# Kernel tuning notes

Measured on AMD Instinct MI355X. Metric: run time of the kernel, lower is better.

The kernel has to match this reference:

```python
import jax, jax.numpy as jnp
import numpy as np

B, S, D, H = 8, 1024, 1024, 16
HD = D // H  # 64


def setup_inputs() -> dict:
    key = jax.random.key(0)
    ks = jax.random.split(key, 10)
    s = 1.0 / np.sqrt(HD)
    x = jax.random.normal(ks[0], (B, S, D), dtype=jnp.float32)
    mask = jax.random.randint(ks[1], (B, S), 0, 2).astype(bool)  # True = padded
    # per-head q/k/v projections of SimpleAttention, stacked over heads
    Wq = jax.random.normal(ks[2], (H, HD, HD), dtype=jnp.float32) * s
    bq = jnp.zeros((H, HD), dtype=jnp.float32)
    Wk = jax.random.normal(ks[3], (H, HD, HD), dtype=jnp.float32) * s
    bk = jnp.zeros((H, HD), dtype=jnp.float32)
    Wv = jax.random.normal(ks[4], (H, HD, HD), dtype=jnp.float32) * s
    bv = jnp.zeros((H, HD), dtype=jnp.float32)
    # out_proj: Linear(dim, dim)
    Wo = jax.random.normal(ks[5], (D, D), dtype=jnp.float32) * (1.0 / np.sqrt(D))
    bo = jnp.zeros((D,), dtype=jnp.float32)
    return {"x": x, "mask": mask, "Wq": Wq, "bq": bq, "Wk": Wk, "bk": bk,
            "Wv": Wv, "bv": bv, "Wo": Wo, "bo": bo}


def reference(x, mask, Wq, bq, Wk, bk, Wv, bv, Wo, bo):
    b, s, d = x.shape
    xh = x.reshape(b, s, H, HD).transpose(0, 2, 1, 3)  # (b, h, s, hd)
    # per-head linear projections (batched over heads via einsum)
    q = jnp.einsum('bhsd,hde->bhse', xh, Wq) + bq[None, :, None, :]
    k = jnp.einsum('bhsd,hde->bhse', xh, Wk) + bk[None, :, None, :]
    v = jnp.einsum('bhsd,hde->bhse', xh, Wv) + bv[None, :, None, :]
    scale = 1.0 / jnp.sqrt(jnp.asarray(HD, dtype=x.dtype))
    scores = jnp.einsum('bhqd,bhkd->bhqk', q, k) * scale  # (b, h, s, s)
    # key-padding mask: True = padded -> -inf on key axis
    neg = jnp.asarray(jnp.finfo(x.dtype).min, dtype=x.dtype)
    scores = jnp.where(mask[:, None, None, :], neg, scores)
    attn = jax.nn.softmax(scores, axis=-1)
    out = jnp.einsum('bhqk,bhkd->bhqd', attn, v)  # (b, h, s, hd)
    concat = out.transpose(0, 2, 1, 3).reshape(b, s, d)
    # out_proj (dropout is identity in eval)
    return concat @ Wo.T + bo
```

## Files before the change

kernel.cpp:

```cpp
#include <hip/hip_runtime.h>
#include <float.h>

#define B_ 8
#define S_ 1024
#define D_ 1024
#define H_ 16
#define HD_ 64

typedef __attribute__((ext_vector_type(8))) _Float16 half8;
typedef __attribute__((ext_vector_type(4))) _Float16 half4;
typedef __attribute__((ext_vector_type(4))) float f32x4;

__device__ __forceinline__ void gld16(const void* g, void* l) {
  __builtin_amdgcn_global_load_lds(
      (const __attribute__((address_space(1))) void*)g,
      (__attribute__((address_space(3))) void*)l, 16, 0, 0);
}

__global__ void detect_mask_kernel(const unsigned int* __restrict__ m, int* __restrict__ flag) {
  __shared__ int bad;
  if (threadIdx.x == 0) bad = 0;
  __syncthreads();
  int my = 0;
  for (int i = threadIdx.x; i < 2048; i += 256) {
    if (m[i] & ~1u) my = 1;
  }
  if (my) atomicOr(&bad, 1);
  __syncthreads();
  if (threadIdx.x == 0) *flag = bad;
}

__global__ void expand_mask_kernel(const unsigned char* __restrict__ mb,
                                   const int* __restrict__ mi,
                                   const int* __restrict__ flag,
                                   float* __restrict__ maskadd) {
  int i = blockIdx.x * 256 + threadIdx.x;
  if (i < B_ * S_) {
    int f = *flag;
    int v = f ? (int)mb[i] : mi[i];
    maskadd[i] = (v != 0) ? -FLT_MAX : 0.0f;
  }
}

__global__ void cast_wo_kernel(const float* __restrict__ Wo, _Float16* __restrict__ Wo16) {
  int i = blockIdx.x * 256 + threadIdx.x;
  if (i < D_ * D_) Wo16[i] = (_Float16)Wo[i];
}

__global__ void cast_wqkv_kernel(const float* __restrict__ Wq, const float* __restrict__ bq,
                                 const float* __restrict__ Wk, const float* __restrict__ bk,
                                 const float* __restrict__ Wv, const float* __restrict__ bv,
                                 _Float16* __restrict__ Wc, float* __restrict__ bs) {
  int idx = blockIdx.x * 256 + threadIdx.x;
  if (idx < 16 * 3 * 64 * 64) {
    int d = idx & 63;
    int e = (idx >> 6) & 63;
    int t2 = idx >> 12;
    int m = t2 % 3, h = t2 / 3;
    int src = h * 4096 + d * 64 + e;
    float v = (m == 0) ? Wq[src] * 0.18033688f : (m == 1) ? Wk[src] : Wv[src];
    Wc[idx] = (_Float16)v;
  }
  if (idx < 3072) {
    int m = idx >> 10, he = idx & 1023;
    float v = (m == 0) ? bq[he] * 0.18033688f : (m == 1) ? bk[he] : bv[he];
    bs[idx] = v;
  }
}

__global__ __launch_bounds__(256) void qkv_kernel(
    const float* __restrict__ x, const _Float16* __restrict__ Wc,
    const float* __restrict__ bs,
    _Float16* __restrict__ q16, _Float16* __restrict__ k16, _Float16* __restrict__ vT16) {
  const int tile = blockIdx.x & 15;
  const int bh = blockIdx.x >> 4;
  const int b = bh >> 4, h = bh & 15;
  const int s0 = tile * 64;
  const int w = threadIdx.x >> 6, lane = threadIdx.x & 63;
  const int col = lane & 15, quad = lane >> 4;
  const int srow = s0 + w * 16 + col;

  const float* xr = x + ((size_t)(b * S_) + srow) * D_ + h * HD_;
  f32x4 x0a = *(const f32x4*)(xr + quad * 8);
  f32x4 x0b = *(const f32x4*)(xr + quad * 8 + 4);
  f32x4 x1a = *(const f32x4*)(xr + 32 + quad * 8);
  f32x4 x1b = *(const f32x4*)(xr + 32 + quad * 8 + 4);
  half8 Xf0, Xf1;
#pragma unroll
  for (int j = 0; j < 4; ++j) {
    Xf0[j] = (_Float16)x0a[j];
    Xf0[4 + j] = (_Float16)x0b[j];
    Xf1[j] = (_Float16)x1a[j];
    Xf1[4 + j] = (_Float16)x1b[j];
  }

  const _Float16* wbase = Wc + (size_t)h * 3 * 4096;
  const f32x4 z4 = {0.f, 0.f, 0.f, 0.f};
#pragma unroll
  for (int mm = 0; mm < 2; ++mm) {
    _Float16* outp = mm ? k16 : q16;
    const _Float16* wm = wbase + mm * 4096;
#pragma unroll
    for (int et = 0; et < 4; ++et) {
      const _Float16* wr = wm + (et * 16 + col) * 64;
      half8 W0 = *(const half8*)(wr + quad * 8);
      half8 W1 = *(const half8*)(wr + 32 + quad * 8);
      f32x4 c = __builtin_amdgcn_mfma_f32_16x16x32_f16(W0, Xf0, z4, 0, 0, 0);
      c = __builtin_amdgcn_mfma_f32_16x16x32_f16(W1, Xf1, c, 0, 0, 0);
      f32x4 bb = *(const f32x4*)(bs + mm * 1024 + h * 64 + et * 16 + quad * 4);
      half4 o;
#pragma unroll
      for (int r = 0; r < 4; ++r) o[r] = (_Float16)(c[r] + bb[r]);
      *(half4*)(outp + ((size_t)bh * S_ + srow) * HD_ + et * 16 + quad * 4) = o;
    }
  }
  {
    const _Float16* wm = wbase + 2 * 4096;
#pragma unroll
    for (int et = 0; et < 4; ++et) {
      const _Float16* wr = wm + (et * 16 + col) * 64;
      half8 W0 = *(const half8*)(wr + quad * 8);
      half8 W1 = *(const half8*)(wr + 32 + quad * 8);
      f32x4 c = __builtin_amdgcn_mfma_f32_16x16x32_f16(Xf0, W0, z4, 0, 0, 0);
      c = __builtin_amdgcn_mfma_f32_16x16x32_f16(Xf1, W1, c, 0, 0, 0);
      float bb = bs[2048 + h * 64 + et * 16 + col];
      half4 o;
#pragma unroll
      for (int r = 0; r < 4; ++r) o[r] = (_Float16)(c[r] + bb);
      *(half4*)(vT16 + ((size_t)bh * HD_ + et * 16 + col) * S_ + s0 + w * 16 + quad * 4) = o;
    }
  }
}

__global__ __launch_bounds__(256, 4) void attn_kernel(
    const _Float16* __restrict__ q, const _Float16* __restrict__ k,
    const _Float16* __restrict__ vT, const float* __restrict__ maskadd,
    _Float16* __restrict__ att) {
  __shared__ alignas(16) _Float16 Ks[2][64 * 64];
  __shared__ alignas(16) _Float16 Vs[2][64 * 64];
  const int bh = blockIdx.x & 127;
  const int qblk = blockIdx.x >> 7;
  const int b = bh >> 4, h = bh & 15;
  const int wv = threadIdx.x >> 6;
  const int lane = threadIdx.x & 63;
  const int quad = lane >> 4, col = lane & 15;
  const int c7 = col & 7;
  const int q0 = qblk * 128 + wv * 32;

  const _Float16* __restrict__ kb = k + (size_t)bh * S_ * HD_;
  const _Float16* __restrict__ vb = vT + (size_t)bh * HD_ * S_;
  const float* __restrict__ mrow = maskadd + b * S_;

  const int jj0 = wv * 128 + lane, jj1 = jj0 + 64;
  const int r0s = jj0 >> 3, r1s = jj1 >> 3;
  const int sg0 = (jj0 & 7) ^ (r0s & 7), sg1 = (jj1 & 7) ^ (r1s & 7);
  const int offK0 = r0s * 128 + sg0 * 16, offK1 = r1s * 128 + sg1 * 16;
  const int offV0 = r0s * 2048 + sg0 * 16, offV1 = r1s * 2048 + sg1 * 16;
  const int ldsb0 = wv * 1024, ldsb1 = wv * 1024 + 512;

  half8 Qf[2][2];
#pragma unroll
  for (int qt = 0; qt < 2; ++qt) {
    const _Float16* qrow = q + ((size_t)bh * S_ + q0 + qt * 16 + col) * HD_;
    Qf[qt][0] = *(const half8*)(qrow + quad * 8);
    Qf[qt][1] = *(const half8*)(qrow + 32 + quad * 8);
  }

  const f32x4 z4 = {0.f, 0.f, 0.f, 0.f};
  f32x4 O[2][4];
#pragma unroll
  for (int qt = 0; qt < 2; ++qt)
#pragma unroll
    for (int et = 0; et < 4; ++et) O[qt][et] = z4;
  float l[2] = {0.f, 0.f};

  {
    const char* kg = (const char*)kb;
    const char* vg = (const char*)vb;
    gld16(kg + offK0, &Ks[0][ldsb0]);
    gld16(kg + offK1, &Ks[0][ldsb1]);
    gld16(vg + offV0, &Vs[0][ldsb0]);
    gld16(vg + offV1, &Vs[0][ldsb1]);
  }
  int cur = 0;
  for (int c = 0; c < 16; ++c) {
    __syncthreads();
    if (c < 15) {
      const char* kg = (const char*)kb + (size_t)(c + 1) * 8192;
      const char* vg = (const char*)vb + (size_t)(c + 1) * 128;
      gld16(kg + offK0, &Ks[cur ^ 1][ldsb0]);
      gld16(kg + offK1, &Ks[cur ^ 1][ldsb1]);
      gld16(vg + offV0, &Vs[cur ^ 1][ldsb0]);
      gld16(vg + offV1, &Vs[cur ^ 1][ldsb1]);
    }
    const int kk0 = c * 64;
    const _Float16* Kb_ = &Ks[cur][0];
    const _Float16* Vb_ = &Vs[cur][0];
    f32x4 mkv[4];
#pragma unroll
    for (int kt = 0; kt < 4; ++kt) mkv[kt] = *(const f32x4*)(mrow + kk0 + kt * 16 + quad * 4);
    half8 Kf[4][2];
#pragma unroll
    for (int kt = 0; kt < 4; ++kt) {
      const int rb = (kt * 16 + col) * 64;
      Kf[kt][0] = *(const half8*)&Kb_[rb + ((quad) ^ c7) * 8];
      Kf[kt][1] = *(const half8*)&Kb_[rb + ((4 + quad) ^ c7) * 8];
    }
    f32x4 st[2][4];
#pragma unroll
    for (int qt = 0; qt < 2; ++qt)
#pragma unroll
      for (int kt = 0; kt < 4; ++kt) {
        f32x4 s = __builtin_amdgcn_mfma_f32_16x16x32_f16(Kf[kt][0], Qf[qt][0], mkv[kt], 0, 0, 0);
        st[qt][kt] = __builtin_amdgcn_mfma_f32_16x16x32_f16(Kf[kt][1], Qf[qt][1], s, 0, 0, 0);
      }
    half4 Vf[4][4];
#pragma unroll
    for (int kt = 0; kt < 4; ++kt) {
      const int sb = ((kt * 2 + (quad >> 1)) ^ c7) * 8 + (quad & 1) * 4;
#pragma unroll
      for (int et = 0; et < 4; ++et) Vf[kt][et] = *(const half4*)&Vb_[(et * 16 + col) * 64 + sb];
    }
#pragma unroll
    for (int qt = 0; qt < 2; ++qt) {
      float p[16];
#pragma unroll
      for (int kt = 0; kt < 4; ++kt)
#pragma unroll
        for (int r = 0; r < 4; ++r) p[kt * 4 + r] = __builtin_amdgcn_exp2f(st[qt][kt][r]);
      float s01 = (p[0] + p[1]) + (p[2] + p[3]);
      float s23 = (p[4] + p[5]) + (p[6] + p[7]);
      float s45 = (p[8] + p[9]) + (p[10] + p[11]);
      float s67 = (p[12] + p[13]) + (p[14] + p[15]);
      l[qt] += (s01 + s23) + (s45 + s67);
      half4 ph[4];
#pragma unroll
      for (int kt = 0; kt < 4; ++kt)
#pragma unroll
        for (int r = 0; r < 4; ++r) ph[kt][r] = (_Float16)p[kt * 4 + r];
#pragma unroll
      for (int et = 0; et < 4; ++et) {
        f32x4 o = O[qt][et];
#pragma unroll
        for (int kt = 0; kt < 4; ++kt)
          o = __builtin_amdgcn_mfma_f32_16x16x16f16(Vf[kt][et], ph[kt], o, 0, 0, 0);
        O[qt][et] = o;
      }
    }
    cur ^= 1;
  }
#pragma unroll
  for (int qt = 0; qt < 2; ++qt) {
    float lt = l[qt];
    lt += __shfl_xor(lt, 16);
    lt += __shfl_xor(lt, 32);
    const float inv = 1.0f / lt;
    _Float16* orow = att + ((size_t)(b * S_ + q0 + qt * 16 + col)) * D_ + h * HD_;
#pragma unroll
    for (int et = 0; et < 4; ++et) {
      half4 o;
#pragma unroll
      for (int r = 0; r < 4; ++r) o[r] = (_Float16)(O[qt][et][r] * inv);
      *(half4*)(orow + et * 16 + quad * 4) = o;
    }
  }
}

__global__ __launch_bounds__(256, 4) void outproj_kernel(
    const _Float16* __restrict__ A, const _Float16* __restrict__ Bw,
    const float* __restrict__ bo, float* __restrict__ C) {
  __shared__ alignas(16) _Float16 As[128 * 64];
  __shared__ alignas(16) _Float16 Bs[128 * 64];
  const int m0 = (int)(blockIdx.x >> 3) * 128;
  const int n0 = (int)(blockIdx.x & 7) * 128;
  const int t = threadIdx.x;
  const int lane = t & 63, wv = t >> 6;
  const int quad = lane >> 4, col = lane & 15;
  const int mw = (wv >> 1) * 64, nw = (wv & 1) * 64;

  int rowS[4], segS[4];
#pragma unroll
  for (int sweep = 0; sweep < 4; ++sweep) {
    const int s = sweep * 256 + wv * 64 + lane;
    rowS[sweep] = s >> 3;
    segS[sweep] = (s & 7) ^ (rowS[sweep] & 7);
  }

  f32x4 acc[16];
  const f32x4 z4 = {0.f, 0.f, 0.f, 0.f};
#pragma unroll
  for (int i = 0; i < 16; ++i) acc[i] = z4;

  for (int kt = 0; kt < 16; ++kt) {
#pragma unroll
    for (int sweep = 0; sweep < 4; ++sweep) {
      const int ldsbase = (sweep * 256 + wv * 64) * 8;
      gld16(A + (size_t)(m0 + rowS[sweep]) * D_ + kt * 64 + segS[sweep] * 8, &As[ldsbase]);
      gld16(Bw + (size_t)(n0 + rowS[sweep]) * D_ + kt * 64 + segS[sweep] * 8, &Bs[ldsbase]);
    }
    __syncthreads();
#pragma unroll
    for (int ks = 0; ks < 2; ++ks) {
      half8 aF[4], bF[4];
#pragma unroll
      for (int mt = 0; mt < 4; ++mt) {
        const int row = mw + mt * 16 + col;
        aF[mt] = *(const half8*)&As[row * 64 + (((ks * 4 + quad) ^ (row & 7)) * 8)];
      }
#pragma unroll
      for (int nt = 0; nt < 4; ++nt) {
        const int row = nw + nt * 16 + col;
        bF[nt] = *(const half8*)&Bs[row * 64 + (((ks * 4 + quad) ^ (row & 7)) * 8)];
      }
#pragma unroll
      for (int mt = 0; mt < 4; ++mt)
#pragma unroll
        for (int nt = 0; nt < 4; ++nt)
          acc[mt * 4 + nt] =
              __builtin_amdgcn_mfma_f32_16x16x32_f16(aF[mt], bF[nt], acc[mt * 4 + nt], 0, 0, 0);
    }
    __syncthreads();
  }
#pragma unroll
  for (int mt = 0; mt < 4; ++mt)
#pragma unroll
    for (int nt = 0; nt < 4; ++nt) {
      f32x4 a = acc[mt * 4 + nt];
      const int n = n0 + nw + nt * 16 + col;
      const float bb = bo[n];
#pragma unroll
      for (int r = 0; r < 4; ++r) {
        const int mrow = m0 + mw + mt * 16 + quad * 4 + r;
        C[(size_t)mrow * D_ + n] = a[r] + bb;
      }
    }
}

extern "C" void kernel_launch(void* const* d_in, const int* in_sizes, int n_in,
                              void* d_out, int out_size, void* d_ws, size_t ws_size,
                              hipStream_t stream) {
  const float* x  = (const float*)d_in[0];
  const float* Wq = (const float*)d_in[2];
  const float* bq = (const float*)d_in[3];
  const float* Wk = (const float*)d_in[4];
  const float* bk = (const float*)d_in[5];
  const float* Wv = (const float*)d_in[6];
  const float* bv = (const float*)d_in[7];
  const float* Wo = (const float*)d_in[8];
  const float* bo = (const float*)d_in[9];

  float* wsf     = (float*)d_ws;
  float* maskadd = wsf;
  int*   flag    = (int*)(wsf + 8192);
  const size_t NE = (size_t)B_ * H_ * S_ * HD_;
  _Float16* hws  = (_Float16*)(wsf + 16384);
  _Float16* q16  = hws;
  _Float16* k16  = q16 + NE;
  _Float16* vT16 = k16 + NE;
  _Float16* att16 = vT16 + NE;
  _Float16* Wo16 = att16 + NE;
  _Float16* Wc   = Wo16 + 1048576;
  float*    bs   = (float*)(Wc + 196608);

  detect_mask_kernel<<<1, 256, 0, stream>>>((const unsigned int*)d_in[1], flag);
  expand_mask_kernel<<<(B_ * S_ + 255) / 256, 256, 0, stream>>>(
      (const unsigned char*)d_in[1], (const int*)d_in[1], flag, maskadd);
  cast_wo_kernel<<<(D_ * D_ + 255) / 256, 256, 0, stream>>>(Wo, Wo16);
  cast_wqkv_kernel<<<(16 * 3 * 64 * 64 + 255) / 256, 256, 0, stream>>>(
      Wq, bq, Wk, bk, Wv, bv, Wc, bs);
  qkv_kernel<<<B_ * H_ * (S_ / 64), 256, 0, stream>>>(x, Wc, bs, q16, k16, vT16);
  attn_kernel<<<B_ * H_ * (S_ / 128), 256, 0, stream>>>(q16, k16, vT16, maskadd, att16);
  outproj_kernel<<<(B_ * S_ / 128) * (D_ / 128), 256, 0, stream>>>(att16, Wo16, bo, (float*)d_out);
}
```

Baseline: 210.2 us.

## Fuse prep kernels into one launch and double attention query tile per block

```diff
diff --git a/kernel.cpp b/kernel.cpp
--- a/kernel.cpp
+++ b/kernel.cpp
@@ -17,54 +17,45 @@
       (__attribute__((address_space(3))) void*)l, 16, 0, 0);
 }
 
-__global__ void detect_mask_kernel(const unsigned int* __restrict__ m, int* __restrict__ flag) {
-  __shared__ int bad;
-  if (threadIdx.x == 0) bad = 0;
-  __syncthreads();
-  int my = 0;
-  for (int i = threadIdx.x; i < 2048; i += 256) {
-    if (m[i] & ~1u) my = 1;
-  }
-  if (my) atomicOr(&bad, 1);
-  __syncthreads();
-  if (threadIdx.x == 0) *flag = bad;
-}
-
-__global__ void expand_mask_kernel(const unsigned char* __restrict__ mb,
-                                   const int* __restrict__ mi,
-                                   const int* __restrict__ flag,
-                                   float* __restrict__ maskadd) {
-  int i = blockIdx.x * 256 + threadIdx.x;
-  if (i < B_ * S_) {
-    int f = *flag;
-    int v = f ? (int)mb[i] : mi[i];
-    maskadd[i] = (v != 0) ? -FLT_MAX : 0.0f;
-  }
-}
-
-__global__ void cast_wo_kernel(const float* __restrict__ Wo, _Float16* __restrict__ Wo16) {
-  int i = blockIdx.x * 256 + threadIdx.x;
-  if (i < D_ * D_) Wo16[i] = (_Float16)Wo[i];
-}
-
-__global__ void cast_wqkv_kernel(const float* __restrict__ Wq, const float* __restrict__ bq,
-                                 const float* __restrict__ Wk, const float* __restrict__ bk,
-                                 const float* __restrict__ Wv, const float* __restrict__ bv,
-                                 _Float16* __restrict__ Wc, float* __restrict__ bs) {
-  int idx = blockIdx.x * 256 + threadIdx.x;
-  if (idx < 16 * 3 * 64 * 64) {
-    int d = idx & 63;
-    int e = (idx >> 6) & 63;
-    int t2 = idx >> 12;
-    int m = t2 % 3, h = t2 / 3;
-    int src = h * 4096 + d * 64 + e;
+__global__ __launch_bounds__(256) void prep_kernel(
+    const float* __restrict__ Wq, const float* __restrict__ bq,
+    const float* __restrict__ Wk, const float* __restrict__ bk,
+    const float* __restrict__ Wv, const float* __restrict__ bv,
+    const float* __restrict__ Wo, const void* __restrict__ mraw,
+    _Float16* __restrict__ Wc, float* __restrict__ bs,
+    _Float16* __restrict__ Wo16, float* __restrict__ maskadd) {
+  const int bid = blockIdx.x;
+  const int tid = threadIdx.x;
+  if (bid < 768) {
+    const int idx = bid * 256 + tid;
+    const int d = idx & 63;
+    const int e = (idx >> 6) & 63;
+    const int t2 = idx >> 12;
+    const int m = t2 % 3, h = t2 / 3;
+    const int src = h * 4096 + d * 64 + e;
     float v = (m == 0) ? Wq[src] * 0.18033688f : (m == 1) ? Wk[src] : Wv[src];
     Wc[idx] = (_Float16)v;
-  }
-  if (idx < 3072) {
-    int m = idx >> 10, he = idx & 1023;
-    float v = (m == 0) ? bq[he] * 0.18033688f : (m == 1) ? bk[he] : bv[he];
-    bs[idx] = v;
+    if (idx < 3072) {
+      const int mm = idx >> 10, he = idx & 1023;
+      float vv = (mm == 0) ? bq[he] * 0.18033688f : (mm == 1) ? bk[he] : bv[he];
+      bs[idx] = vv;
+    }
+  } else if (bid < 800) {
+    __shared__ int bad;
+    if (tid == 0) bad = 0;
+    __syncthreads();
+    const unsigned int* mw = (const unsigned int*)mraw;
+    int my = 0;
+    for (int j = tid; j < 2048; j += 256) my |= (mw[j] & ~1u) ? 1 : 0;
+    if (my) atomicOr(&bad, 1);
+    __syncthreads();
+    const int i = (bid - 768) * 256 + tid;
+    const int f = bad;
+    const int v = f ? (int)((const unsigned char*)mraw)[i] : ((const int*)mraw)[i];
+    maskadd[i] = (v != 0) ? -FLT_MAX : 0.0f;
+  } else {
+    const int i = (bid - 800) * 256 + tid;
+    Wo16[i] = (_Float16)Wo[i];
   }
 }
 
@@ -132,7 +123,7 @@
   }
 }
 
-__global__ __launch_bounds__(256, 4) void attn_kernel(
+__global__ __launch_bounds__(256, 2) void attn_kernel(
     const _Float16* __restrict__ q, const _Float16* __restrict__ k,
     const _Float16* __restrict__ vT, const float* __restrict__ maskadd,
     _Float16* __restrict__ att) {
@@ -145,7 +136,7 @@
   const int lane = threadIdx.x & 63;
   const int quad = lane >> 4, col = lane & 15;
   const int c7 = col & 7;
-  const int q0 = qblk * 128 + wv * 32;
+  const int q0 = qblk * 256 + wv * 64;
 
   const _Float16* __restrict__ kb = k + (size_t)bh * S_ * HD_;
   const _Float16* __restrict__ vb = vT + (size_t)bh * HD_ * S_;
@@ -158,21 +149,21 @@
   const int offV0 = r0s * 2048 + sg0 * 16, offV1 = r1s * 2048 + sg1 * 16;
   const int ldsb0 = wv * 1024, ldsb1 = wv * 1024 + 512;
 
-  half8 Qf[2][2];
-#pragma unroll
-  for (int qt = 0; qt < 2; ++qt) {
+  half8 Qf[4][2];
+#pragma unroll
+  for (int qt = 0; qt < 4; ++qt) {
     const _Float16* qrow = q + ((size_t)bh * S_ + q0 + qt * 16 + col) * HD_;
     Qf[qt][0] = *(const half8*)(qrow + quad * 8);
     Qf[qt][1] = *(const half8*)(qrow + 32 + quad * 8);
   }
 
   const f32x4 z4 = {0.f, 0.f, 0.f, 0.f};
-  f32x4 O[2][4];
-#pragma unroll
-  for (int qt = 0; qt < 2; ++qt)
+  f32x4 O[4][4];
+#pragma unroll
+  for (int qt = 0; qt < 4; ++qt)
 #pragma unroll
     for (int et = 0; et < 4; ++et) O[qt][et] = z4;
-  float l[2] = {0.f, 0.f};
+  float l[4] = {0.f, 0.f, 0.f, 0.f};
 
   {
     const char* kg = (const char*)kb;
@@ -206,28 +197,26 @@
       Kf[kt][0] = *(const half8*)&Kb_[rb + ((quad) ^ c7) * 8];
       Kf[kt][1] = *(const half8*)&Kb_[rb + ((4 + quad) ^ c7) * 8];
     }
-    f32x4 st[2][4];
-#pragma unroll
-    for (int qt = 0; qt < 2; ++qt)
+    half4 Vf[4][4];
+#pragma unroll
+    for (int kt = 0; kt < 4; ++kt) {
+      const int sb = ((kt * 2 + (quad >> 1)) ^ c7) * 8 + (quad & 1) * 4;
+#pragma unroll
+      for (int et = 0; et < 4; ++et) Vf[kt][et] = *(const half4*)&Vb_[(et * 16 + col) * 64 + sb];
+    }
+#pragma unroll
+    for (int qt = 0; qt < 4; ++qt) {
+      f32x4 st[4];
 #pragma unroll
       for (int kt = 0; kt < 4; ++kt) {
         f32x4 s = __builtin_amdgcn_mfma_f32_16x16x32_f16(Kf[kt][0], Qf[qt][0], mkv[kt], 0, 0, 0);
-        st[qt][kt] = __builtin_amdgcn_mfma_f32_16x16x32_f16(Kf[kt][1], Qf[qt][1], s, 0, 0, 0);
-      }
-    half4 Vf[4][4];
-#pragma unroll
-    for (int kt = 0; kt < 4; ++kt) {
-      const int sb = ((kt * 2 + (quad >> 1)) ^ c7) * 8 + (quad & 1) * 4;
-#pragma unroll
-      for (int et = 0; et < 4; ++et) Vf[kt][et] = *(const half4*)&Vb_[(et * 16 + col) * 64 + sb];
-    }
-#pragma unroll
-    for (int qt = 0; qt < 2; ++qt) {
+        st[kt] = __builtin_amdgcn_mfma_f32_16x16x32_f16(Kf[kt][1], Qf[qt][1], s, 0, 0, 0);
+      }
       float p[16];
 #pragma unroll
       for (int kt = 0; kt < 4; ++kt)
 #pragma unroll
-        for (int r = 0; r < 4; ++r) p[kt * 4 + r] = __builtin_amdgcn_exp2f(st[qt][kt][r]);
+        for (int r = 0; r < 4; ++r) p[kt * 4 + r] = __builtin_amdgcn_exp2f(st[kt][r]);
       float s01 = (p[0] + p[1]) + (p[2] + p[3]);
       float s23 = (p[4] + p[5]) + (p[6] + p[7]);
       float s45 = (p[8] + p[9]) + (p[10] + p[11]);
@@ -250,7 +239,7 @@
     cur ^= 1;
   }
 #pragma unroll
-  for (int qt = 0; qt < 2; ++qt) {
+  for (int qt = 0; qt < 4; ++qt) {
     float lt = l[qt];
     lt += __shfl_xor(lt, 16);
     lt += __shfl_xor(lt, 32);
@@ -351,7 +340,6 @@
 
   float* wsf     = (float*)d_ws;
   float* maskadd = wsf;
-  int*   flag    = (int*)(wsf + 8192);
   const size_t NE = (size_t)B_ * H_ * S_ * HD_;
   _Float16* hws  = (_Float16*)(wsf + 16384);
   _Float16* q16  = hws;
@@ -362,13 +350,9 @@
   _Float16* Wc   = Wo16 + 1048576;
   float*    bs   = (float*)(Wc + 196608);
 
-  detect_mask_kernel<<<1, 256, 0, stream>>>((const unsigned int*)d_in[1], flag);
-  expand_mask_kernel<<<(B_ * S_ + 255) / 256, 256, 0, stream>>>(
-      (const unsigned char*)d_in[1], (const int*)d_in[1], flag, maskadd);
-  cast_wo_kernel<<<(D_ * D_ + 255) / 256, 256, 0, stream>>>(Wo, Wo16);
-  cast_wqkv_kernel<<<(16 * 3 * 64 * 64 + 255) / 256, 256, 0, stream>>>(
-      Wq, bq, Wk, bk, Wv, bv, Wc, bs);
+  prep_kernel<<<4896, 256, 0, stream>>>(Wq, bq, Wk, bk, Wv, bv, Wo, d_in[1],
+                                        Wc, bs, Wo16, maskadd);
   qkv_kernel<<<B_ * H_ * (S_ / 64), 256, 0, stream>>>(x, Wc, bs, q16, k16, vT16);
-  attn_kernel<<<B_ * H_ * (S_ / 128), 256, 0, stream>>>(q16, k16, vT16, maskadd, att16);
+  attn_kernel<<<B_ * H_ * (S_ / 256), 256, 0, stream>>>(q16, k16, vT16, maskadd, att16);
   outproj_kernel<<<(B_ * S_ / 128) * (D_ / 128), 256, 0, stream>>>(att16, Wo16, bo, (float*)d_out);
 }
```

Result: faster. 199.2 us (-5.2%).
